# Performance work log

Hardware: AMD Instinct MI355X
Metric: run time of the kernel (lower is better)

Reference implementation:

```python
import jax, jax.numpy as jnp
import numpy as np

B, S_IMG, S_TXT, P, D, HEADS, HD = 1, 2048, 512, 4, 3072, 24, 128


def rmsnorm(x, weight=None, eps=1e-6):
    var = jnp.mean(jnp.square(x), axis=-1, keepdims=True)
    y = x * jax.lax.rsqrt(var + eps)
    return y * weight if weight is not None else y


def apply_rope(x, cos, sin):
    # x: [B,H,S,Dh]; cos/sin: [S,Dh]; interleaved real/imag rotation (diffusers use_real_unbind_dim=-1)
    xr = x.reshape(*x.shape[:-1], -1, 2)
    rot = jnp.stack([-xr[..., 1], xr[..., 0]], axis=-1).reshape(x.shape)
    return x * cos[None, None] + rot * sin[None, None]


def sdpa(q, k, v):
    scores = jnp.einsum('bhqd,bhkd->bhqk', q, k) / jnp.sqrt(jnp.asarray(q.shape[-1], q.dtype))
    return jnp.einsum('bhqk,bhkd->bhqd', jax.nn.softmax(scores, axis=-1), v)


def heads_split(x):
    # [B,S,D] -> [B,H,S,Dh]
    return x.reshape(x.shape[0], x.shape[1], HEADS, HD).transpose(0, 2, 1, 3)


def heads_merge(x):
    # [B,H,S,Dh] -> [B,S,D]
    return x.transpose(0, 2, 1, 3).reshape(x.shape[0], x.shape[2], HEADS * HD)


def setup_inputs() -> dict:
    key = jax.random.key(0)
    ks = jax.random.split(key, 32)
    init = lambda k, shape: (jax.random.normal(k, shape, dtype=jnp.float32) * 0.02)
    inp = {
        'hidden_states': jax.random.normal(ks[0], (B, S_IMG, D), dtype=jnp.float32),
        'encoder_hidden_states': jax.random.normal(ks[1], (B, S_TXT, D), dtype=jnp.float32),
        'ip_encoder_hidden_states': jax.random.normal(ks[2], (B, P, D), dtype=jnp.float32),
        'layer_scale': jax.random.uniform(ks[3], (B,), dtype=jnp.float32),
        'Wq': init(ks[4], (D, D)), 'bq': jnp.zeros((D,), jnp.float32),
        'Wk': init(ks[5], (D, D)), 'bk': jnp.zeros((D,), jnp.float32),
        'Wv': init(ks[6], (D, D)), 'bv': jnp.zeros((D,), jnp.float32),
        'norm_q_w': jnp.ones((HD,), jnp.float32),
        'norm_k_w': jnp.ones((HD,), jnp.float32),
        'Waq': init(ks[7], (D, D)), 'baq': jnp.zeros((D,), jnp.float32),
        'Wak': init(ks[8], (D, D)), 'bak': jnp.zeros((D,), jnp.float32),
        'Wav': init(ks[9], (D, D)), 'bav': jnp.zeros((D,), jnp.float32),
        'norm_aq_w': jnp.ones((HD,), jnp.float32),
        'norm_ak_w': jnp.ones((HD,), jnp.float32),
        'Wk_ip': init(ks[10], (D, D)),
        'Wv_ip': init(ks[11], (D, D)),
        'Wo': init(ks[12], (D, D)), 'bo': jnp.zeros((D,), jnp.float32),
        'Wao': init(ks[13], (D, D)), 'bao': jnp.zeros((D,), jnp.float32),
    }
    # rotary cos/sin over the joint (text+image) sequence, interleaved freqs per diffusers FLUX
    pos = jnp.arange(S_TXT + S_IMG, dtype=jnp.float32)
    inv_freq = 1.0 / (10000.0 ** (jnp.arange(0, HD, 2, dtype=jnp.float32) / HD))
    angles = pos[:, None] * inv_freq[None, :]            # [S, HD/2]
    angles = jnp.repeat(angles, 2, axis=-1)              # [S, HD]
    inp['cos'] = jnp.cos(angles)
    inp['sin'] = jnp.sin(angles)
    return inp


IP_SCALE = 1.0  # self.scale


def reference(hidden_states, encoder_hidden_states, ip_encoder_hidden_states, cos, sin,
              layer_scale, Wq, bq, Wk, bk, Wv, bv, norm_q_w, norm_k_w,
              Waq, baq, Wak, bak, Wav, bav, norm_aq_w, norm_ak_w,
              Wk_ip, Wv_ip, Wo, bo, Wao, bao):
    # image-stream projections
    q = heads_split(hidden_states @ Wq.T + bq)
    k = heads_split(hidden_states @ Wk.T + bk)
    v = heads_split(hidden_states @ Wv.T + bv)
    q = rmsnorm(q, norm_q_w, 1e-6)
    k = rmsnorm(k, norm_k_w, 1e-6)

    # IP-adapter cross-attention (queries = image tokens, kv = IP tokens)
    ip_k = rmsnorm(heads_split(ip_encoder_hidden_states @ Wk_ip.T), None, 1e-5)
    ip_v = heads_split(ip_encoder_hidden_states @ Wv_ip.T)
    ip_out = heads_merge(sdpa(q, ip_k, ip_v))            # [B, S_img, D]

    # text (encoder) stream projections, prepended to joint sequence
    eq = rmsnorm(heads_split(encoder_hidden_states @ Waq.T + baq), norm_aq_w, 1e-6)
    ek = rmsnorm(heads_split(encoder_hidden_states @ Wak.T + bak), norm_ak_w, 1e-6)
    ev = heads_split(encoder_hidden_states @ Wav.T + bav)
    q = jnp.concatenate([eq, q], axis=2)
    k = jnp.concatenate([ek, k], axis=2)
    v = jnp.concatenate([ev, v], axis=2)

    q = apply_rope(q, cos, sin)
    k = apply_rope(k, cos, sin)

    out = heads_merge(sdpa(q, k, v))                     # [B, S_txt+S_img, D]
    n_txt = encoder_hidden_states.shape[1]
    enc_out, img_out = out[:, :n_txt], out[:, n_txt:]

    ls = layer_scale.reshape(-1, 1, 1)
    img_out = img_out + IP_SCALE * ls * ip_out
    img_out = img_out @ Wo.T + bo
    enc_out = enc_out @ Wao.T + bao
    return (img_out, enc_out)
```

## Files before the change

### kernel.cpp

```cpp
#include <hip/hip_runtime.h>

typedef _Float16 half_t;
typedef _Float16 half2v __attribute__((ext_vector_type(2)));
typedef _Float16 half4v __attribute__((ext_vector_type(4)));
typedef _Float16 half8v __attribute__((ext_vector_type(8)));
typedef float    float4v __attribute__((ext_vector_type(4)));
typedef short    short8v __attribute__((ext_vector_type(8)));

#define S_IMG 2048
#define S_TXT 512
#define S_TOT 2560
#define NH    24
#define HD    128
#define DM    3072

__device__ __forceinline__ void gload16(const void* g, void* l) {
  __builtin_amdgcn_global_load_lds(
      (const __attribute__((address_space(1))) unsigned int*)g,
      (__attribute__((address_space(3))) unsigned int*)l, 16, 0, 0);
}

__global__ void cvt_act_kernel(const float* __restrict__ hs, const float* __restrict__ enc,
                               half_t* __restrict__ d) {
  const long NHS = (long)S_IMG * DM;
  const long TOT = NHS + (long)S_TXT * DM;
  long i = ((long)blockIdx.x * 256 + threadIdx.x) * 8;
  long stride = (long)gridDim.x * 256 * 8;
  for (; i < TOT; i += stride) {
    const float* s = i < NHS ? hs + i : enc + (i - NHS);
    float4v v0 = *(const float4v*)(s);
    float4v v1 = *(const float4v*)(s + 4);
    half8v h;
    h[0] = (half_t)v0[0]; h[1] = (half_t)v0[1]; h[2] = (half_t)v0[2]; h[3] = (half_t)v0[3];
    h[4] = (half_t)v1[0]; h[5] = (half_t)v1[1]; h[6] = (half_t)v1[2]; h[7] = (half_t)v1[3];
    *(half8v*)(d + i) = h;
  }
}

__global__ void cvt3_kernel(const float* __restrict__ s0, const float* __restrict__ s1,
                            const float* __restrict__ s2,
                            half_t* __restrict__ d0, half_t* __restrict__ d1,
                            half_t* __restrict__ d2, int n) {
  const float* s = blockIdx.y == 0 ? s0 : (blockIdx.y == 1 ? s1 : s2);
  half_t* d = blockIdx.y == 0 ? d0 : (blockIdx.y == 1 ? d1 : d2);
  int i = (blockIdx.x * 256 + threadIdx.x) * 8;
  int stride = gridDim.x * 256 * 8;
  for (; i < n; i += stride) {
    float4v v0 = *(const float4v*)(s + i);
    float4v v1 = *(const float4v*)(s + i + 4);
    half8v h;
    h[0] = (half_t)v0[0]; h[1] = (half_t)v0[1]; h[2] = (half_t)v0[2]; h[3] = (half_t)v0[3];
    h[4] = (half_t)v1[0]; h[5] = (half_t)v1[1]; h[6] = (half_t)v1[2]; h[7] = (half_t)v1[3];
    *(half8v*)(d + i) = h;
  }
}

template <typename OUT>
__device__ __forceinline__ void gemm_tile(half_t* As, half_t* Bs,
                                          const half_t* __restrict__ A,
                                          const half_t* __restrict__ Bt,
                                          const float* __restrict__ bias,
                                          OUT* __restrict__ C, int bm, int bn) {
  const int K = DM, N = DM;
  const int tid = threadIdx.x, wid = tid >> 6, l = tid & 63;
  const int wm = (wid >> 1) * 64, wn = (wid & 1) * 64;
  const int l15 = l & 15, l4 = l >> 4;
  float4v acc[4][4] = {};

  const int scol = ((l & 3) ^ ((l >> 3) & 3)) * 8;
  const half_t* ga = A + (long)(bm + wid * 32 + (l >> 2)) * K + scol;
  const half_t* gb = Bt + (long)(bn + wid * 32 + (l >> 2)) * K + scol;
  const long rowstep = 16l * K;

#define GSTAGE(T, SEL)                                                        \
  {                                                                           \
    char* a_d = (char*)As + (SEL) * 8192 + wid * 2048;                        \
    char* b_d = (char*)Bs + (SEL) * 8192 + wid * 2048;                        \
    int k0 = (T) * 32;                                                        \
    gload16(ga + k0, a_d);                                                    \
    gload16(ga + rowstep + k0, a_d + 1024);                                   \
    gload16(gb + k0, b_d);                                                    \
    gload16(gb + rowstep + k0, b_d + 1024);                                   \
  }

  GSTAGE(0, 0);
  GSTAGE(1, 1);

  const int NT = K / 32;
  const int cofs = (l4 * 16) ^ (((l15 >> 1) & 3) << 4);
  for (int t = 0; t < NT; t++) {
    int cur = t % 3;
    if (t + 1 < NT) asm volatile("s_waitcnt vmcnt(4)" ::: "memory");
    else            asm volatile("s_waitcnt vmcnt(0)" ::: "memory");
    __builtin_amdgcn_s_barrier();
    __builtin_amdgcn_sched_barrier(0);
    if (t + 2 < NT) GSTAGE(t + 2, (t + 2) % 3);
    __builtin_amdgcn_sched_barrier(0);
    const char* AsB = (const char*)As + cur * 8192;
    const char* BsB = (const char*)Bs + cur * 8192;
    half8v af[4], bf[4];
#pragma unroll
    for (int i = 0; i < 4; i++)
      af[i] = *(const half8v*)(AsB + (wm + i * 16 + l15) * 64 + cofs);
#pragma unroll
    for (int j = 0; j < 4; j++)
      bf[j] = *(const half8v*)(BsB + (wn + j * 16 + l15) * 64 + cofs);
    __builtin_amdgcn_s_setprio(1);
#pragma unroll
    for (int i = 0; i < 4; i++)
#pragma unroll
      for (int j = 0; j < 4; j++)
        acc[i][j] = __builtin_amdgcn_mfma_f32_16x16x32_f16(af[i], bf[j], acc[i][j], 0, 0, 0);
    __builtin_amdgcn_s_setprio(0);
  }
#undef GSTAGE
#pragma unroll
  for (int i = 0; i < 4; i++)
#pragma unroll
    for (int j = 0; j < 4; j++) {
      int row = bm + wm + i * 16 + l4 * 4;
      int col = bn + wn + j * 16 + l15;
      float bv = bias ? bias[col] : 0.0f;
#pragma unroll
      for (int r = 0; r < 4; r++) {
        float v = acc[i][j][r] + bv;
        C[(long)(row + r) * N + col] = (OUT)v;
      }
    }
}

template <int NROW>
__global__ __launch_bounds__(256) void gemm3_kernel(const half_t* __restrict__ A,
                                                    const half_t* __restrict__ W0,
                                                    const half_t* __restrict__ W1,
                                                    const half_t* __restrict__ W2,
                                                    const float* b0, const float* b1, const float* b2,
                                                    half_t* O0, half_t* O1, half_t* O2) {
  __shared__ half_t As[3 * 128 * 32];
  __shared__ half_t Bs[3 * 128 * 32];
  int b = blockIdx.x;
  int q = (72 * NROW) >> 3;
  int wg = (b & 7) * q + (b >> 3);
  int col = wg / NROW, row = wg % NROW;
  int sel = col / 24;
  const half_t* Bt = sel == 0 ? W0 : (sel == 1 ? W1 : W2);
  const float* bias = sel == 0 ? b0 : (sel == 1 ? b1 : b2);
  half_t* C = sel == 0 ? O0 : (sel == 1 ? O1 : O2);
  gemm_tile<half_t>(As, Bs, A, Bt, bias, C, row * 128, (col % 24) * 128);
}

__global__ __launch_bounds__(256) void gemm_out_kernel(const half_t* __restrict__ ocomb,
                                                       const half_t* __restrict__ Wo_h,
                                                       const half_t* __restrict__ Wao_h,
                                                       const float* bo, const float* bao,
                                                       float* out_img, float* out_enc) {
  __shared__ half_t As[3 * 128 * 32];
  __shared__ half_t Bs[3 * 128 * 32];
  int b = blockIdx.x;
  int wg = (b & 7) * 60 + (b >> 3);
  int col = wg / 20, r = wg % 20;
  bool enc = r >= 16;
  const half_t* A = enc ? ocomb : ocomb + (long)S_TXT * DM;
  int bm = (enc ? (r - 16) : r) * 128;
  gemm_tile<float>(As, Bs, A, enc ? Wao_h : Wo_h, enc ? bao : bo,
                   enc ? out_enc : out_img, bm, col * 128);
}

__global__ __launch_bounds__(256) void ip_proj_kernel(const float* __restrict__ x,
                                                      const float* __restrict__ Wk_ip,
                                                      const float* __restrict__ Wv_ip,
                                                      float* __restrict__ outk,
                                                      float* __restrict__ outv) {
  const float* W = blockIdx.y ? Wv_ip : Wk_ip;
  float* out = blockIdx.y ? outv : outk;
  int n = blockIdx.x * 4 + (threadIdx.x >> 6);
  int l = threadIdx.x & 63;
  const float* wr = W + (long)n * DM;
  float acc[4] = {0.f, 0.f, 0.f, 0.f};
  for (int k = l * 4; k < DM; k += 256) {
    float4v wv = *(const float4v*)(wr + k);
#pragma unroll
    for (int p = 0; p < 4; p++) {
      float4v xv = *(const float4v*)(x + p * DM + k);
      acc[p] += wv[0] * xv[0] + wv[1] * xv[1] + wv[2] * xv[2] + wv[3] * xv[3];
    }
  }
#pragma unroll
  for (int off = 32; off; off >>= 1)
#pragma unroll
    for (int p = 0; p < 4; p++) acc[p] += __shfl_xor(acc[p], off, 64);
  if (l == 0)
#pragma unroll
    for (int p = 0; p < 4; p++) out[p * DM + n] = acc[p];
}

__global__ void ip_norm_kernel(const float* __restrict__ kr, const float* __restrict__ vr,
                               half_t* __restrict__ kh, half_t* __restrict__ vh) {
  int t = blockIdx.x;
  int l = threadIdx.x;
  int d = l * 2;
  if (t < 96) {
    int base = (t / 24) * DM + (t % 24) * HD;
    float x0 = kr[base + d], x1 = kr[base + d + 1];
    float ss = x0 * x0 + x1 * x1;
#pragma unroll
    for (int off = 32; off; off >>= 1) ss += __shfl_xor(ss, off, 64);
    float r = rsqrtf(ss * (1.0f / HD) + 1e-5f);
    kh[base + d] = (half_t)(x0 * r);
    kh[base + d + 1] = (half_t)(x1 * r);
  } else {
    int t2 = t - 96;
    int base = (t2 / 24) * DM + (t2 % 24) * HD;
    vh[base + d] = (half_t)vr[base + d];
    vh[base + d + 1] = (half_t)vr[base + d + 1];
  }
}

__global__ __launch_bounds__(256) void prep_kernel(
    const half_t* __restrict__ qraw, const half_t* __restrict__ kraw,
    const half_t* __restrict__ eq, const half_t* __restrict__ ek,
    const float* __restrict__ nqw, const float* __restrict__ nkw,
    const float* __restrict__ naqw, const float* __restrict__ nakw,
    const float* __restrict__ cosb, const float* __restrict__ sinb,
    half_t* __restrict__ qcat, half_t* __restrict__ kcat, half_t* __restrict__ qnr) {
  int task = blockIdx.x * 4 + (threadIdx.x >> 6);
  int l = threadIdx.x & 63;
  int s = task / NH, h = task - (task / NH) * NH;
  int d = l * 2;
  const half_t *qs, *ks;
  const float *wq, *wk;
  if (s < S_TXT) {
    long base = (long)s * DM + h * HD;
    qs = eq + base; ks = ek + base;
    wq = naqw; wk = nakw;
  } else {
    long base = (long)(s - S_TXT) * DM + h * HD;
    qs = qraw + base; ks = kraw + base;
    wq = nqw; wk = nkw;
  }
  half2v qv = *(const half2v*)(qs + d);
  half2v kv = *(const half2v*)(ks + d);
  float q0 = (float)qv[0], q1 = (float)qv[1];
  float k0 = (float)kv[0], k1 = (float)kv[1];
  float ssq = q0 * q0 + q1 * q1;
  float ssk = k0 * k0 + k1 * k1;
#pragma unroll
  for (int off = 32; off; off >>= 1) {
    ssq += __shfl_xor(ssq, off, 64);
    ssk += __shfl_xor(ssk, off, 64);
  }
  float rq = rsqrtf(ssq * (1.0f / HD) + 1e-6f);
  float rk = rsqrtf(ssk * (1.0f / HD) + 1e-6f);
  float qn0 = q0 * rq * wq[d], qn1 = q1 * rq * wq[d + 1];
  float kn0 = k0 * rk * wk[d], kn1 = k1 * rk * wk[d + 1];
  if (s >= S_TXT) {
    half2v o; o[0] = (half_t)qn0; o[1] = (half_t)qn1;
    *(half2v*)(qnr + ((long)h * S_IMG + (s - S_TXT)) * HD + d) = o;
  }
  float c0 = cosb[s * HD + d], c1 = cosb[s * HD + d + 1];
  float s0 = sinb[s * HD + d], s1 = sinb[s * HD + d + 1];
  float qo0 = qn0 * c0 - qn1 * s0, qo1 = qn1 * c1 + qn0 * s1;
  float ko0 = kn0 * c0 - kn1 * s0, ko1 = kn1 * c1 + kn0 * s1;
  long ci = ((long)h * S_TOT + s) * HD + d;
  half2v oq; oq[0] = (half_t)qo0; oq[1] = (half_t)qo1;
  half2v ok; ok[0] = (half_t)ko0; ok[1] = (half_t)ko1;
  *(half2v*)(qcat + ci) = oq;
  *(half2v*)(kcat + ci) = ok;
}

__global__ __launch_bounds__(256) void vtrans_kernel(const half_t* __restrict__ ev,
                                                     const half_t* __restrict__ vraw,
                                                     half_t* __restrict__ vcatT) {
  __shared__ half_t T[64][136];
  int h = blockIdx.y, sb = blockIdx.x * 64;
  int t = threadIdx.x;
#pragma unroll
  for (int i = 0; i < 4; i++) {
    int c = t + i * 256;
    int row = c >> 4, col = (c & 15) * 8;
    int s = sb + row;
    const half_t* src = (s < S_TXT) ? ev + (long)s * DM + h * HD + col
                                    : vraw + (long)(s - S_TXT) * DM + h * HD + col;
    *(half8v*)&T[row][col] = *(const half8v*)src;
  }
  __syncthreads();
#pragma unroll
  for (int i = 0; i < 4; i++) {
    int c = t + i * 256;
    int d = c >> 3, sc = (c & 7) * 8;
    half8v v;
#pragma unroll
    for (int j = 0; j < 8; j++) v[j] = T[sc + j][d];
    int base = (sc & 32) | ((sc & 8) << 1) | ((sc & 16) >> 2);
    half_t* dst = vcatT + ((long)h * HD + d) * S_TOT + sb;
    half4v q0; q0[0] = v[0]; q0[1] = v[1]; q0[2] = v[2]; q0[3] = v[3];
    half4v q1; q1[0] = v[4]; q1[1] = v[5]; q1[2] = v[6]; q1[3] = v[7];
    *(half4v*)(dst + base) = q0;
    *(half4v*)(dst + base + 8) = q1;
  }
}

__global__ __launch_bounds__(256) void ip_attn_kernel(const half_t* __restrict__ qnr,
                                                      const half_t* __restrict__ kh,
                                                      const half_t* __restrict__ vh,
                                                      half_t* __restrict__ ipout) {
  int tid = threadIdx.x;
  int task = blockIdx.x * 16 + (tid >> 4);
  int l16 = tid & 15;
  int h = task >> 11;
  int s = task & 2047;
  int d = l16 * 8;
  half8v qv = *(const half8v*)(qnr + ((long)h * S_IMG + s) * HD + d);
  float sc[4];
#pragma unroll
  for (int p = 0; p < 4; p++) {
    half8v kv = *(const half8v*)(kh + p * DM + h * HD + d);
    float a = 0.f;
#pragma unroll
    for (int j = 0; j < 8; j++) a += (float)qv[j] * (float)kv[j];
    sc[p] = a;
  }
#pragma unroll
  for (int off = 8; off; off >>= 1)
#pragma unroll
    for (int p = 0; p < 4; p++) sc[p] += __shfl_xor(sc[p], off, 16);
  float m = fmaxf(fmaxf(sc[0], sc[1]), fmaxf(sc[2], sc[3]));
  float e[4], sum = 0.f;
#pragma unroll
  for (int p = 0; p < 4; p++) { e[p] = __expf((sc[p] - m) * 0.088388347648318447f); sum += e[p]; }
  float inv = 1.0f / sum;
  float o[8] = {};
#pragma unroll
  for (int p = 0; p < 4; p++) {
    half8v vv = *(const half8v*)(vh + p * DM + h * HD + d);
#pragma unroll
    for (int j = 0; j < 8; j++) o[j] += e[p] * (float)vv[j];
  }
  half8v ov;
#pragma unroll
  for (int j = 0; j < 8; j++) ov[j] = (half_t)(o[j] * inv);
  *(half8v*)(ipout + (long)s * DM + h * HD + d) = ov;
}

__global__ __launch_bounds__(256, 2) void flash_kernel(const half_t* __restrict__ qcat,
                                                       const half_t* __restrict__ kcat,
                                                       const half_t* __restrict__ vcatT,
                                                       const half_t* __restrict__ ipout,
                                                       const float* __restrict__ lsp,
                                                       half_t* __restrict__ ocomb) {
  __shared__ half_t Ks[2 * 64 * 128];
  __shared__ half_t Vs[2 * 128 * 64];
  int b = blockIdx.x;
  int wg = (b & 7) * 60 + (b >> 3);
  const int h = wg / 20, qb = wg % 20;
  const int tid = threadIdx.x, wid = tid >> 6, l = tid & 63;
  const int l15 = l & 15, l4 = l >> 4;
  const float CEXP = 0.12754137969983614f;

  half8v qf[2][4];
#pragma unroll
  for (int t = 0; t < 2; t++) {
    int qrow = qb * 128 + wid * 32 + t * 16 + l15;
    const half_t* qp = qcat + ((long)h * S_TOT + qrow) * HD;
#pragma unroll
    for (int kk = 0; kk < 4; kk++) qf[t][kk] = *(const half8v*)(qp + kk * 32 + l4 * 8);
  }
  float4v o[2][8] = {};
  float lsum[2] = {0.f, 0.f};
  const float ls = lsp[0];

  const char* kb = (const char*)(kcat + (long)h * S_TOT * HD);
  const char* vb = (const char*)(vcatT + (long)h * HD * S_TOT);
  int kof[4];
  long vof[4];
#pragma unroll
  for (int c = 0; c < 4; c++) {
    int L = c * 4096 + tid * 16;
    kof[c] = L ^ (((L >> 8) & 7) << 4);
    int vrow = L >> 7;
    vof[c] = (long)vrow * (S_TOT * 2) + ((L & 127) ^ ((vrow & 7) << 4));
  }

#define STAGE(KT, SEL)                                                        \
  {                                                                           \
    char* kd = (char*)Ks + (SEL) * 16384 + wid * 1024;                        \
    char* vd = (char*)Vs + (SEL) * 16384 + wid * 1024;                        \
    _Pragma("unroll") for (int c = 0; c < 4; c++) {                           \
      gload16(kb + (long)(KT) * 256 + kof[c], kd + c * 4096);                 \
      gload16(vb + vof[c] + (KT) * 2, vd + c * 4096);                         \
    }                                                                         \
  }

  STAGE(0, 0);

  const int NT = S_TOT / 64;
  int sel = 0;
  for (int it = 0; it < NT; it++) {
    asm volatile("s_waitcnt vmcnt(0)" ::: "memory");
    __builtin_amdgcn_s_barrier();
    __builtin_amdgcn_sched_barrier(0);
    if (it + 1 < NT) STAGE((it + 1) * 64, sel ^ 1);

    const char* KsB = (const char*)Ks + sel * 16384;
    const char* VsB = (const char*)Vs + sel * 16384;

    float4v s0[4] = {}, s1[4] = {};
    __builtin_amdgcn_s_setprio(1);
#pragma unroll
    for (int nb = 0; nb < 4; nb++) {
      int krow = nb * 16 + l15;
      int rb = krow << 8;
      int sw = (krow & 7) << 4;
#pragma unroll
      for (int kk = 0; kk < 4; kk++) {
        half8v kf = *(const half8v*)(KsB + rb + ((kk * 64 + l4 * 16) ^ sw));
        s0[nb] = __builtin_amdgcn_mfma_f32_16x16x32_f16(kf, qf[0][kk], s0[nb], 0, 0, 0);
        s1[nb] = __builtin_amdgcn_mfma_f32_16x16x32_f16(kf, qf[1][kk], s1[nb], 0, 0, 0);
      }
    }
    __builtin_amdgcn_s_setprio(0);
    half8v pa00, pa01, pa10, pa11;
    {
      float sum0 = 0.f, sum1 = 0.f;
      float e0[4][4], e1[4][4];
#pragma unroll
      for (int nb = 0; nb < 4; nb++)
#pragma unroll
        for (int r = 0; r < 4; r++) {
          float a = exp2f(s0[nb][r] * CEXP - 2.0f);
          float c = exp2f(s1[nb][r] * CEXP - 2.0f);
          e0[nb][r] = a; e1[nb][r] = c;
          sum0 += a; sum1 += c;
        }
      lsum[0] += sum0; lsum[1] += sum1;
#pragma unroll
      for (int r = 0; r < 4; r++) {
        pa00[r] = (half_t)e0[0][r]; pa00[r + 4] = (half_t)e0[1][r];
        pa01[r] = (half_t)e0[2][r]; pa01[r + 4] = (half_t)e0[3][r];
        pa10[r] = (half_t)e1[0][r]; pa10[r + 4] = (half_t)e1[1][r];
        pa11[r] = (half_t)e1[2][r]; pa11[r + 4] = (half_t)e1[3][r];
      }
    }
    __builtin_amdgcn_s_setprio(1);
#pragma unroll
    for (int cb = 0; cb < 8; cb++) {
      int row = cb * 16 + l15;
      int sw = (row & 7) << 4;
      half8v vf0 = *(const half8v*)(VsB + (row << 7) + ((l4 * 16) ^ sw));
      half8v vf1 = *(const half8v*)(VsB + (row << 7) + ((64 + l4 * 16) ^ sw));
      o[0][cb] = __builtin_amdgcn_mfma_f32_16x16x32_f16(pa00, vf0, o[0][cb], 0, 0, 0);
      o[0][cb] = __builtin_amdgcn_mfma_f32_16x16x32_f16(pa01, vf1, o[0][cb], 0, 0, 0);
      o[1][cb] = __builtin_amdgcn_mfma_f32_16x16x32_f16(pa10, vf0, o[1][cb], 0, 0, 0);
      o[1][cb] = __builtin_amdgcn_mfma_f32_16x16x32_f16(pa11, vf1, o[1][cb], 0, 0, 0);
    }
    __builtin_amdgcn_s_setprio(0);
    sel ^= 1;
  }
#undef STAGE
  float lreg[2];
#pragma unroll
  for (int t = 0; t < 2; t++) {
    float s = lsum[t];
    s += __shfl_xor(s, 16, 64);
    s += __shfl_xor(s, 32, 64);
    lreg[t] = s;
  }
#pragma unroll
  for (int t = 0; t < 2; t++) {
    float invq = 1.0f / lreg[t];
#pragma unroll
    for (int r = 0; r < 4; r++) {
      float inv = __shfl(invq, l4 * 4 + r, 64);
      int s = qb * 128 + wid * 32 + t * 16 + l4 * 4 + r;
#pragma unroll
      for (int cb = 0; cb < 8; cb++) {
        int col = h * HD + cb * 16 + l15;
        float val = o[t][cb][r] * inv;
        if (s >= S_TXT) val += ls * (float)ipout[(long)(s - S_TXT) * DM + col];
        ocomb[(long)s * DM + col] = (half_t)val;
      }
    }
  }
}

extern "C" void kernel_launch(void* const* d_in, const int* in_sizes, int n_in,
                              void* d_out, int out_size, void* d_ws, size_t ws_size,
                              hipStream_t stream) {
  (void)in_sizes; (void)n_in; (void)out_size; (void)ws_size;
  const float* hs    = (const float*)d_in[0];
  const float* enc   = (const float*)d_in[1];
  const float* ipenc = (const float*)d_in[2];
  const float* lsc   = (const float*)d_in[3];
  const float* Wq  = (const float*)d_in[4];  const float* bq  = (const float*)d_in[5];
  const float* Wk  = (const float*)d_in[6];  const float* bk  = (const float*)d_in[7];
  const float* Wv  = (const float*)d_in[8];  const float* bv  = (const float*)d_in[9];
  const float* nqw = (const float*)d_in[10]; const float* nkw = (const float*)d_in[11];
  const float* Waq = (const float*)d_in[12]; const float* baq = (const float*)d_in[13];
  const float* Wak = (const float*)d_in[14]; const float* bak = (const float*)d_in[15];
  const float* Wav = (const float*)d_in[16]; const float* bav = (const float*)d_in[17];
  const float* naqw= (const float*)d_in[18]; const float* nakw= (const float*)d_in[19];
  const float* Wkip= (const float*)d_in[20]; const float* Wvip= (const float*)d_in[21];
  const float* Wo  = (const float*)d_in[22]; const float* bo  = (const float*)d_in[23];
  const float* Wao = (const float*)d_in[24]; const float* bao = (const float*)d_in[25];
  const float* cosb= (const float*)d_in[26]; const float* sinb= (const float*)d_in[27];

  const size_t WSZ = (size_t)DM * DM;
  const size_t HSZ = (size_t)S_IMG * DM;
  const size_t ESZ = (size_t)S_TXT * DM;
  const size_t CSZ = (size_t)NH * S_TOT * HD;

  half_t* base = (half_t*)d_ws;
  half_t* W3    = base;
  half_t* hs_h  = W3 + 3 * WSZ;
  half_t* enc_h = hs_h + HSZ;
  half_t* qkvr  = enc_h + ESZ;
  half_t* eqkv  = qkvr + 3 * HSZ;
  half_t* qcat  = eqkv + 3 * ESZ;
  half_t* kcat  = qcat + CSZ;
  half_t* vcatT = kcat + CSZ;

  half_t* q_raw = qkvr;
  half_t* k_raw = qkvr + HSZ;
  half_t* v_raw = qkvr + 2 * HSZ;
  half_t* eq_r  = eqkv;
  half_t* ek_r  = eqkv + ESZ;
  half_t* ev_r  = eqkv + 2 * ESZ;
  half_t* qnr   = hs_h;
  half_t* ipout = qkvr;
  half_t* ocomb = qkvr + HSZ;
  float*  ipk_raw = (float*)enc_h;
  float*  ipv_raw = ipk_raw + 4 * DM;
  half_t* ipk_h  = enc_h + 16 * DM;
  half_t* ipv_h  = ipk_h + 4 * DM;

  cvt_act_kernel<<<2048, 256, 0, stream>>>(hs, enc, hs_h);

  cvt3_kernel<<<dim3(1024, 3), 256, 0, stream>>>(Wq, Wk, Wv, W3, W3 + WSZ, W3 + 2 * WSZ, (int)WSZ);
  gemm3_kernel<16><<<1152, 256, 0, stream>>>(hs_h, W3, W3 + WSZ, W3 + 2 * WSZ,
                                             bq, bk, bv, q_raw, k_raw, v_raw);
  cvt3_kernel<<<dim3(1024, 3), 256, 0, stream>>>(Waq, Wak, Wav, W3, W3 + WSZ, W3 + 2 * WSZ, (int)WSZ);
  gemm3_kernel<4><<<288, 256, 0, stream>>>(enc_h, W3, W3 + WSZ, W3 + 2 * WSZ,
                                           baq, bak, bav, eq_r, ek_r, ev_r);
  ip_proj_kernel<<<dim3(768, 2), 256, 0, stream>>>(ipenc, Wkip, Wvip, ipk_raw, ipv_raw);
  ip_norm_kernel<<<192, 64, 0, stream>>>(ipk_raw, ipv_raw, ipk_h, ipv_h);

  prep_kernel<<<(S_TOT * NH) / 4, 256, 0, stream>>>(q_raw, k_raw, eq_r, ek_r,
                                                    nqw, nkw, naqw, nakw, cosb, sinb,
                                                    qcat, kcat, qnr);
  vtrans_kernel<<<dim3(S_TOT / 64, NH), 256, 0, stream>>>(ev_r, v_raw, vcatT);

  ip_attn_kernel<<<(NH * S_IMG) / 16, 256, 0, stream>>>(qnr, ipk_h, ipv_h, ipout);

  flash_kernel<<<480, 256, 0, stream>>>(qcat, kcat, vcatT, ipout, lsc, ocomb);

  float* out_img = (float*)d_out;
  float* out_enc = (float*)d_out + (size_t)S_IMG * DM;
  cvt3_kernel<<<dim3(1024, 2), 256, 0, stream>>>(Wo, Wao, Wao, W3, W3 + WSZ, W3 + 2 * WSZ, (int)WSZ);
  gemm_out_kernel<<<480, 256, 0, stream>>>(ocomb, W3, W3 + WSZ, bo, bao, out_img, out_enc);
}
```

Baseline: 555.6 us.

## Merge weight conversions and QKV GEMMs, overlap output-weight cast with flash

When the workspace is large enough, all six QKV weight matrices and the activations are converted to fp16 in one launch. Both the image and text QKV projections then run as a single 1440-block GEMM launch, where the two separate GEMMs each had a partial last wave. The Wo/Wao fp32-to-fp16 conversion moves into extra blocks of the flash attention launch so it runs alongside attention instead of as its own kernel. This removes several launches and fills tail waves, at the cost of a larger workspace and flash blocks competing with conversion blocks for bandwidth and CUs.

```diff
diff --git a/kernel.cpp b/kernel.cpp
--- a/kernel.cpp
+++ b/kernel.cpp
@@ -13,6 +13,9 @@
 #define NH    24
 #define HD    128
 #define DM    3072
+#define WSZC  9437184L
+#define HSZC  6291456L
+#define ESZC  1572864L
 
 __device__ __forceinline__ void gload16(const void* g, void* l) {
   __builtin_amdgcn_global_load_lds(
@@ -20,20 +23,29 @@
       (__attribute__((address_space(3))) unsigned int*)l, 16, 0, 0);
 }
 
+__device__ __forceinline__ void cvt8span(const float* s, half_t* d, long i) {
+  float4v v0 = *(const float4v*)(s + i);
+  float4v v1 = *(const float4v*)(s + i + 4);
+  half8v h;
+  h[0] = (half_t)v0[0]; h[1] = (half_t)v0[1]; h[2] = (half_t)v0[2]; h[3] = (half_t)v0[3];
+  h[4] = (half_t)v1[0]; h[5] = (half_t)v1[1]; h[6] = (half_t)v1[2]; h[7] = (half_t)v1[3];
+  *(half8v*)(d + i) = h;
+}
+
 __global__ void cvt_act_kernel(const float* __restrict__ hs, const float* __restrict__ enc,
                                half_t* __restrict__ d) {
-  const long NHS = (long)S_IMG * DM;
-  const long TOT = NHS + (long)S_TXT * DM;
+  const long TOT = HSZC + ESZC;
   long i = ((long)blockIdx.x * 256 + threadIdx.x) * 8;
   long stride = (long)gridDim.x * 256 * 8;
   for (; i < TOT; i += stride) {
-    const float* s = i < NHS ? hs + i : enc + (i - NHS);
+    const float* s = i < HSZC ? hs + i : enc + (i - HSZC);
+    half_t* dd = d + i;
     float4v v0 = *(const float4v*)(s);
     float4v v1 = *(const float4v*)(s + 4);
     half8v h;
     h[0] = (half_t)v0[0]; h[1] = (half_t)v0[1]; h[2] = (half_t)v0[2]; h[3] = (half_t)v0[3];
     h[4] = (half_t)v1[0]; h[5] = (half_t)v1[1]; h[6] = (half_t)v1[2]; h[7] = (half_t)v1[3];
-    *(half8v*)(d + i) = h;
+    *(half8v*)dd = h;
   }
 }
 
@@ -43,16 +55,28 @@
                             half_t* __restrict__ d2, int n) {
   const float* s = blockIdx.y == 0 ? s0 : (blockIdx.y == 1 ? s1 : s2);
   half_t* d = blockIdx.y == 0 ? d0 : (blockIdx.y == 1 ? d1 : d2);
-  int i = (blockIdx.x * 256 + threadIdx.x) * 8;
-  int stride = gridDim.x * 256 * 8;
-  for (; i < n; i += stride) {
-    float4v v0 = *(const float4v*)(s + i);
-    float4v v1 = *(const float4v*)(s + i + 4);
-    half8v h;
-    h[0] = (half_t)v0[0]; h[1] = (half_t)v0[1]; h[2] = (half_t)v0[2]; h[3] = (half_t)v0[3];
-    h[4] = (half_t)v1[0]; h[5] = (half_t)v1[1]; h[6] = (half_t)v1[2]; h[7] = (half_t)v1[3];
-    *(half8v*)(d + i) = h;
-  }
+  long i = ((long)blockIdx.x * 256 + threadIdx.x) * 8;
+  long stride = (long)gridDim.x * 256 * 8;
+  for (; i < n; i += stride) cvt8span(s, d, i);
+}
+
+__global__ void cvt8_kernel(const float* w0, const float* w1, const float* w2,
+                            const float* w3, const float* w4, const float* w5,
+                            const float* hs, const float* enc,
+                            half_t* __restrict__ W6, half_t* __restrict__ hs_h) {
+  int y = blockIdx.y;
+  const float* s;
+  half_t* d;
+  long n;
+  if (y < 6) {
+    s = y == 0 ? w0 : y == 1 ? w1 : y == 2 ? w2 : y == 3 ? w3 : y == 4 ? w4 : w5;
+    d = W6 + (long)y * WSZC;
+    n = WSZC;
+  } else if (y == 6) { s = hs; d = hs_h; n = HSZC; }
+  else               { s = enc; d = hs_h + HSZC; n = ESZC; }
+  long i = ((long)blockIdx.x * 256 + threadIdx.x) * 8;
+  long stride = (long)gridDim.x * 256 * 8;
+  for (; i < n; i += stride) cvt8span(s, d, i);
 }
 
 template <typename OUT>
@@ -127,6 +151,41 @@
         C[(long)(row + r) * N + col] = (OUT)v;
       }
     }
+}
+
+__global__ __launch_bounds__(256) void gemm_qkv_kernel(
+    const half_t* __restrict__ hs_h, const half_t* __restrict__ enc_h,
+    const half_t* __restrict__ W6,
+    const float* bq, const float* bk, const float* bv,
+    const float* baq, const float* bak, const float* bav,
+    half_t* q_raw, half_t* k_raw, half_t* v_raw,
+    half_t* eq_r, half_t* ek_r, half_t* ev_r) {
+  __shared__ half_t As[3 * 4096];
+  __shared__ half_t Bs[3 * 4096];
+  int b = blockIdx.x;
+  int wg = (b & 7) * 180 + (b >> 3);
+  const half_t* A;
+  const half_t* Bt;
+  const float* bias;
+  half_t* C;
+  int bm, bn;
+  if (wg < 1152) {
+    int col = wg / 16, row = wg % 16;
+    int sel = col / 24;
+    A = hs_h; bm = row * 128; bn = (col % 24) * 128;
+    Bt = W6 + (long)sel * WSZC;
+    bias = sel == 0 ? bq : (sel == 1 ? bk : bv);
+    C = sel == 0 ? q_raw : (sel == 1 ? k_raw : v_raw);
+  } else {
+    int w2 = wg - 1152;
+    int col = w2 / 4, row = w2 % 4;
+    int sel = col / 24;
+    A = enc_h; bm = row * 128; bn = (col % 24) * 128;
+    Bt = W6 + (long)(3 + sel) * WSZC;
+    bias = sel == 0 ? baq : (sel == 1 ? bak : bav);
+    C = sel == 0 ? eq_r : (sel == 1 ? ek_r : ev_r);
+  }
+  gemm_tile<half_t>(As, Bs, A, Bt, bias, C, bm, bn);
 }
 
 template <int NROW>
@@ -347,9 +406,23 @@
                                                        const half_t* __restrict__ vcatT,
                                                        const half_t* __restrict__ ipout,
                                                        const float* __restrict__ lsp,
-                                                       half_t* __restrict__ ocomb) {
+                                                       half_t* __restrict__ ocomb,
+                                                       const float* __restrict__ WoF,
+                                                       const float* __restrict__ WaoF,
+                                                       half_t* __restrict__ w0d,
+                                                       half_t* __restrict__ w1d) {
   __shared__ half_t Ks[2 * 64 * 128];
   __shared__ half_t Vs[2 * 128 * 64];
+  if (blockIdx.x >= 480) {
+    int cb = blockIdx.x - 480;
+    long i = ((long)cb * 256 + threadIdx.x) * 8;
+    long stride = (long)(gridDim.x - 480) * 256 * 8;
+    for (; i < 2 * WSZC; i += stride) {
+      if (i < WSZC) cvt8span(WoF, w0d, i);
+      else          cvt8span(WaoF, w1d, i - WSZC);
+    }
+    return;
+  }
   int b = blockIdx.x;
   int wg = (b & 7) * 60 + (b >> 3);
   const int h = wg / 20, qb = wg % 20;
@@ -486,7 +559,7 @@
 extern "C" void kernel_launch(void* const* d_in, const int* in_sizes, int n_in,
                               void* d_out, int out_size, void* d_ws, size_t ws_size,
                               hipStream_t stream) {
-  (void)in_sizes; (void)n_in; (void)out_size; (void)ws_size;
+  (void)in_sizes; (void)n_in; (void)out_size;
   const float* hs    = (const float*)d_in[0];
   const float* enc   = (const float*)d_in[1];
   const float* ipenc = (const float*)d_in[2];
@@ -504,14 +577,17 @@
   const float* Wao = (const float*)d_in[24]; const float* bao = (const float*)d_in[25];
   const float* cosb= (const float*)d_in[26]; const float* sinb= (const float*)d_in[27];
 
-  const size_t WSZ = (size_t)DM * DM;
-  const size_t HSZ = (size_t)S_IMG * DM;
-  const size_t ESZ = (size_t)S_TXT * DM;
+  const size_t WSZ = WSZC;
+  const size_t HSZ = HSZC;
+  const size_t ESZ = ESZC;
   const size_t CSZ = (size_t)NH * S_TOT * HD;
+  const size_t REST = HSZ + ESZ + 3 * HSZ + 3 * ESZ + 3 * CSZ;
+  const bool big = ws_size >= (6 * WSZ + REST) * sizeof(half_t);
+  const int NSLOT = big ? 6 : 3;
 
   half_t* base = (half_t*)d_ws;
-  half_t* W3    = base;
-  half_t* hs_h  = W3 + 3 * WSZ;
+  half_t* Wsl   = base;
+  half_t* hs_h  = Wsl + NSLOT * WSZ;
   half_t* enc_h = hs_h + HSZ;
   half_t* qkvr  = enc_h + ESZ;
   half_t* eqkv  = qkvr + 3 * HSZ;
@@ -533,14 +609,22 @@
   half_t* ipk_h  = enc_h + 16 * DM;
   half_t* ipv_h  = ipk_h + 4 * DM;
 
-  cvt_act_kernel<<<2048, 256, 0, stream>>>(hs, enc, hs_h);
-
-  cvt3_kernel<<<dim3(1024, 3), 256, 0, stream>>>(Wq, Wk, Wv, W3, W3 + WSZ, W3 + 2 * WSZ, (int)WSZ);
-  gemm3_kernel<16><<<1152, 256, 0, stream>>>(hs_h, W3, W3 + WSZ, W3 + 2 * WSZ,
-                                             bq, bk, bv, q_raw, k_raw, v_raw);
-  cvt3_kernel<<<dim3(1024, 3), 256, 0, stream>>>(Waq, Wak, Wav, W3, W3 + WSZ, W3 + 2 * WSZ, (int)WSZ);
-  gemm3_kernel<4><<<288, 256, 0, stream>>>(enc_h, W3, W3 + WSZ, W3 + 2 * WSZ,
-                                           baq, bak, bav, eq_r, ek_r, ev_r);
+  if (big) {
+    cvt8_kernel<<<dim3(1024, 8), 256, 0, stream>>>(Wq, Wk, Wv, Waq, Wak, Wav,
+                                                   hs, enc, Wsl, hs_h);
+    gemm_qkv_kernel<<<1440, 256, 0, stream>>>(hs_h, enc_h, Wsl,
+                                              bq, bk, bv, baq, bak, bav,
+                                              q_raw, k_raw, v_raw, eq_r, ek_r, ev_r);
+  } else {
+    cvt_act_kernel<<<2048, 256, 0, stream>>>(hs, enc, hs_h);
+    cvt3_kernel<<<dim3(1024, 3), 256, 0, stream>>>(Wq, Wk, Wv, Wsl, Wsl + WSZ, Wsl + 2 * WSZ, (int)WSZ);
+    gemm3_kernel<16><<<1152, 256, 0, stream>>>(hs_h, Wsl, Wsl + WSZ, Wsl + 2 * WSZ,
+                                               bq, bk, bv, q_raw, k_raw, v_raw);
+    cvt3_kernel<<<dim3(1024, 3), 256, 0, stream>>>(Waq, Wak, Wav, Wsl, Wsl + WSZ, Wsl + 2 * WSZ, (int)WSZ);
+    gemm3_kernel<4><<<288, 256, 0, stream>>>(enc_h, Wsl, Wsl + WSZ, Wsl + 2 * WSZ,
+                                             baq, bak, bav, eq_r, ek_r, ev_r);
+  }
+
   ip_proj_kernel<<<dim3(768, 2), 256, 0, stream>>>(ipenc, Wkip, Wvip, ipk_raw, ipv_raw);
   ip_norm_kernel<<<192, 64, 0, stream>>>(ipk_raw, ipv_raw, ipk_h, ipv_h);
 
@@ -551,10 +635,16 @@
 
   ip_attn_kernel<<<(NH * S_IMG) / 16, 256, 0, stream>>>(qnr, ipk_h, ipv_h, ipout);
 
-  flash_kernel<<<480, 256, 0, stream>>>(qcat, kcat, vcatT, ipout, lsc, ocomb);
+  if (big) {
+    flash_kernel<<<480 + 512, 256, 0, stream>>>(qcat, kcat, vcatT, ipout, lsc, ocomb,
+                                                Wo, Wao, Wsl, Wsl + WSZ);
+  } else {
+    flash_kernel<<<480, 256, 0, stream>>>(qcat, kcat, vcatT, ipout, lsc, ocomb,
+                                          Wo, Wao, Wsl, Wsl + WSZ);
+    cvt3_kernel<<<dim3(1024, 2), 256, 0, stream>>>(Wo, Wao, Wao, Wsl, Wsl + WSZ, Wsl + 2 * WSZ, (int)WSZ);
+  }
 
   float* out_img = (float*)d_out;
   float* out_enc = (float*)d_out + (size_t)S_IMG * DM;
-  cvt3_kernel<<<dim3(1024, 2), 256, 0, stream>>>(Wo, Wao, Wao, W3, W3 + WSZ, W3 + 2 * WSZ, (int)WSZ);
-  gemm_out_kernel<<<480, 256, 0, stream>>>(ocomb, W3, W3 + WSZ, bo, bao, out_img, out_enc);
-}
+  gemm_out_kernel<<<480, 256, 0, stream>>>(ocomb, Wsl, Wsl + WSZ, bo, bao, out_img, out_enc);
+}
```

Measured after the change: 503.8 us. 9.3% less time.
